# Optimization experiments

Hardware: AMD Instinct MI355X
Metric: run time of the kernel (lower is better)

The kernel has to match this reference:

```python
import jax, jax.numpy as jnp
import numpy as np

B, T, IN, D = 32, 1024, 1536, 768


def setup_inputs() -> dict:
    key = jax.random.key(0)
    ks = jax.random.split(key, 14)
    s_in = 1.0 / np.sqrt(IN)
    s_d = 1.0 / np.sqrt(D)
    return {
        "x": jax.random.normal(ks[0], (B, T, IN), jnp.float32),
        # fc1/fc2 torch Linear weights stored [out, in]
        "fc1_w": jax.random.normal(ks[1], (IN, IN), jnp.float32) * s_in,
        "fc1_b": jax.random.normal(ks[2], (IN,), jnp.float32) * 0.01,
        "fc2_w": jax.random.normal(ks[3], (D, IN), jnp.float32) * s_in,
        "fc2_b": jax.random.normal(ks[4], (D,), jnp.float32) * 0.01,
        # Unary: Conv1d(D,D,k=1) then Conv1d(D,1,k=1); k=1 conv == per-token linear
        "un_emb_w": jax.random.normal(ks[5], (D, D), jnp.float32) * s_d,
        "un_emb_b": jax.random.normal(ks[6], (D,), jnp.float32) * 0.01,
        "un_red_w": jax.random.normal(ks[7], (1, D), jnp.float32) * s_d,
        "un_red_b": jax.random.normal(ks[8], (1,), jnp.float32) * 0.01,
        # Self Pairwise: x_embedding / y_embedding Conv1d(D,D,k=1)
        "pw_x_w": jax.random.normal(ks[9], (D, D), jnp.float32) * s_d,
        "pw_x_b": jax.random.normal(ks[10], (D,), jnp.float32) * 0.01,
        "pw_y_w": jax.random.normal(ks[11], (D, D), jnp.float32) * s_d,
        "pw_y_b": jax.random.normal(ks[12], (D,), jnp.float32) * 0.01,
        # reduce_potentials: Conv1d(2,1,k=1,bias=False) -> 2 scalars
        "red_w": jax.random.normal(ks[13], (2,), jnp.float32),
    }


def reference(x, fc1_w, fc1_b, fc2_w, fc2_b,
              un_emb_w, un_emb_b, un_red_w, un_red_b,
              pw_x_w, pw_x_b, pw_y_w, pw_y_b, red_w):
    # FGAEmbedder MLP: fc2(relu(fc1(x)))
    h = jax.nn.relu(jnp.einsum('bti,oi->bto', x, fc1_w) + fc1_b)
    u = jnp.einsum('bti,oi->bto', h, fc2_w) + fc2_b            # [B,T,D]

    # Unary potential (dropout is identity at inference)
    e = jax.nn.relu(jnp.einsum('btd,od->bto', u, un_emb_w) + un_emb_b)
    un_pot = (jnp.einsum('btd,od->bto', e, un_red_w) + un_red_b)[..., 0]  # [B,T]

    # Self pairwise: cosine-similarity matrix, marginalized by mean (spatial_dim=None)
    xe = jnp.einsum('btd,od->bto', u, pw_x_w) + pw_x_b
    ye = jnp.einsum('btd,od->bto', u, pw_y_w) + pw_y_b
    xn = xe / jnp.maximum(jnp.linalg.norm(xe, axis=-1, keepdims=True), 1e-12)
    yn = ye / jnp.maximum(jnp.linalg.norm(ye, axis=-1, keepdims=True), 1e-12)
    S = jnp.einsum('btd,bsd->bts', xn, yn)                     # [B,T,T]
    pw_pot = jnp.mean(S, axis=2)                               # [B,T]

    # reduce potentials (Conv1d 2->1 no bias; order: unary then self), softmax attention
    scores = red_w[0] * un_pot + red_w[1] * pw_pot             # [B,T]
    w = jax.nn.softmax(scores, axis=1)
    return jnp.einsum('btd,bt->bd', u, w)                      # [B,D]
```

## Files before the change

### kernel.cpp

```cpp
#include <hip/hip_runtime.h>
#include <stdint.h>

#define MROWS 32768
#define TSEQ  1024
#define BBATCH 32
#define INDIM 1536
#define DDIM  768
#define NCAT  2304

typedef short short8 __attribute__((ext_vector_type(8)));
typedef short short4v __attribute__((ext_vector_type(4)));
typedef float f32x4  __attribute__((ext_vector_type(4)));

__device__ __forceinline__ float b2f(ushort u) {
    union { uint32_t u; float f; } x; x.u = ((uint32_t)u) << 16; return x.f;
}
__device__ __forceinline__ ushort f2b(float f) {
    union { float f; uint32_t u; } x; x.f = f;
    uint32_t r = x.u + 0x7fffu + ((x.u >> 16) & 1u);
    return (ushort)(r >> 16);
}

__device__ __forceinline__ void cvt4(const float* __restrict__ in, ushort* __restrict__ out, int i) {
    float4 v = ((const float4*)in)[i];
    ushort4 o;
    o.x = f2b(v.x); o.y = f2b(v.y); o.z = f2b(v.z); o.w = f2b(v.w);
    ((ushort4*)out)[i] = o;
}

#define C0 12582912
#define C1 13172736
#define C2 13467648
#define C3 13615104
#define C4 13762560
#define C5 13910016
#define C6 13910592
#define C7 13916736
#define C8 13922880
#define C9 13947456
__global__ void cvt_all(const float* __restrict__ x,
                        const float* __restrict__ fc1_w, const float* __restrict__ fc2_w,
                        const float* __restrict__ w3a, const float* __restrict__ w3b,
                        const float* __restrict__ w3c,
                        const float* __restrict__ ba, const float* __restrict__ bb,
                        const float* __restrict__ bc,
                        ushort* __restrict__ X16, ushort* __restrict__ W1,
                        ushort* __restrict__ W2, ushort* __restrict__ W3,
                        float* __restrict__ B3, float* __restrict__ ybar_z,
                        float* __restrict__ out_z, float* __restrict__ stats_z)
{
    int i = blockIdx.x * 256 + threadIdx.x;
    float4 z = {0.f, 0.f, 0.f, 0.f};
    if (i < C0)       cvt4(x, X16, i);
    else if (i < C1)  cvt4(fc1_w, W1, i - C0);
    else if (i < C2)  cvt4(fc2_w, W2, i - C1);
    else if (i < C3)  cvt4(w3a, W3,           i - C2);
    else if (i < C4)  cvt4(w3b, W3 + 589824,  i - C3);
    else if (i < C5)  cvt4(w3c, W3 + 1179648, i - C4);
    else if (i < C6) {
        int j = i - C5;
        const float* src = (j < 192) ? ba : (j < 384) ? bb : bc;
        int off = (j < 192) ? j : (j < 384) ? (j - 192) : (j - 384);
        ((float4*)B3)[j] = ((const float4*)src)[off];
    }
    else if (i < C7)  ((float4*)ybar_z)[i - C6] = z;
    else if (i < C8)  ((float4*)out_z)[i - C7] = z;
    else if (i < C9)  ((float4*)stats_z)[i - C8] = z;
}

__global__ __launch_bounds__(512, 2)
void gemm_bt(const ushort* __restrict__ A, const ushort* __restrict__ Bm,
             const float* __restrict__ bias, ushort* __restrict__ C,
             int M, int N, int K, int relu_ncols,
             const float* __restrict__ urw, float* __restrict__ SE,
             float* __restrict__ SX, float* __restrict__ SY)
{
    __shared__ __align__(16) ushort lds[81920];

    const int tid  = threadIdx.x;
    const int lane = tid & 63, wave = tid >> 6;
    const int wm = wave >> 2, wn = wave & 3;
    const int quad = lane >> 4, r16 = lane & 15;

    const int ntiles = N >> 8;
    const int xcd = blockIdx.x & 7;
    const int j   = blockIdx.x >> 3;
    const int g   = j / ntiles;
    const int n_t = j - g * ntiles;
    const int m_t = xcd + (g << 3);
    const int m0 = m_t * 256, n0 = n_t * 256;

    const int srow = lane >> 2;
    const int g8   = (((lane & 3) ^ ((srow >> 1) & 3)) << 3);
    const int goff = (r16 << 5) + ((quad ^ ((r16 >> 1) & 3)) << 3);

    const ushort* pA = A + (size_t)(m0 + (wave & 3) * 16 + srow + (wave >> 2) * 128) * K + g8;
    const int segA = (((wave >> 2) * 8 + (wave & 3)) << 9) + lane * 8;
    const ushort* pB = Bm + (size_t)(n0 + (wave >> 1) * 64 + (wave & 1) * 16 + srow) * K + g8;
    const int segB = (((wave >> 1) * 4 + (wave & 1)) << 9) + lane * 8;

    const int kT = K >> 6;

#define STG(p, off) __builtin_amdgcn_global_load_lds( \
        (const __attribute__((address_space(1))) void*)(p), \
        (__attribute__((address_space(3))) void*)&lds[off], 16, 0, 0)
#define STAGE_A(tt, MH) do { \
        const ushort* s_ = pA + (size_t)(MH) * 64 * K + (size_t)(tt) * 64; \
        const int d_ = ((tt) % 3) * 16384 + (MH) * 2048 + segA; \
        STG(s_,      d_); \
        STG(s_ + 32, d_ + 8192); } while (0)
#define STAGE_B(tt, NH) do { \
        const ushort* s_ = pB + (size_t)(NH) * 32 * K + (size_t)(tt) * 64; \
        const int d_ = 49152 + ((tt) & 1) * 16384 + (NH) * 1024 + segB; \
        STG(s_,      d_); \
        STG(s_ + 32, d_ + 8192); } while (0)

    STAGE_A(0, 0); STAGE_A(0, 1);
    STAGE_B(0, 0); STAGE_B(0, 1);
    STAGE_A(1, 0); STAGE_A(1, 1);
    asm volatile("s_waitcnt vmcnt(4)" ::: "memory");
    asm volatile("s_barrier" ::: "memory");

    f32x4 acc[8][4] = {};

    for (int t = 0; t < kT; ++t) {
        const int aB = (t % 3) * 16384;
        const int bB = 49152 + (t & 1) * 16384;
        short8 af0[2][4], af1[2][4], bf[2][4];

#pragma unroll
        for (int ks = 0; ks < 2; ++ks) {
#pragma unroll
            for (int i = 0; i < 4; ++i)
                af0[ks][i] = *(const short8*)&lds[aB + ks * 8192 + (wm * 8 + i) * 512 + goff];
#pragma unroll
            for (int jj = 0; jj < 4; ++jj)
                bf[ks][jj] = *(const short8*)&lds[bB + ks * 8192 + (wn * 4 + jj) * 512 + goff];
        }
        if (t + 1 < kT) { STAGE_B(t + 1, 0); STAGE_B(t + 1, 1); }
        if (t + 2 < kT) { STAGE_A(t + 2, 0); STAGE_A(t + 2, 1); }

        __builtin_amdgcn_s_setprio(1);
#pragma unroll
        for (int i = 0; i < 4; ++i)
#pragma unroll
            for (int jj = 0; jj < 4; ++jj) {
                acc[i][jj] = __builtin_amdgcn_mfma_f32_16x16x32_bf16(af0[0][i], bf[0][jj], acc[i][jj], 0, 0, 0);
                acc[i][jj] = __builtin_amdgcn_mfma_f32_16x16x32_bf16(af0[1][i], bf[1][jj], acc[i][jj], 0, 0, 0);
            }
        __builtin_amdgcn_s_setprio(0);

#pragma unroll
        for (int ks = 0; ks < 2; ++ks)
#pragma unroll
            for (int i = 0; i < 4; ++i)
                af1[ks][i] = *(const short8*)&lds[aB + ks * 8192 + (wm * 8 + 4 + i) * 512 + goff];

        __builtin_amdgcn_s_setprio(1);
#pragma unroll
        for (int i = 0; i < 4; ++i)
#pragma unroll
            for (int jj = 0; jj < 4; ++jj) {
                acc[4 + i][jj] = __builtin_amdgcn_mfma_f32_16x16x32_bf16(af1[0][i], bf[0][jj], acc[4 + i][jj], 0, 0, 0);
                acc[4 + i][jj] = __builtin_amdgcn_mfma_f32_16x16x32_bf16(af1[1][i], bf[1][jj], acc[4 + i][jj], 0, 0, 0);
            }
        __builtin_amdgcn_s_setprio(0);

        if (t + 2 < kT)      asm volatile("s_waitcnt vmcnt(4)" ::: "memory");
        else if (t + 1 < kT) asm volatile("s_waitcnt vmcnt(0)" ::: "memory");
        if (t + 1 < kT)      asm volatile("s_barrier" ::: "memory");
    }
#undef STAGE_A
#undef STAGE_B
#undef STG

    const bool stats = (urw != nullptr);
    const int sec = n0 / DDIM;
    float bv[4], uwv[4];
    bool dr[4];
#pragma unroll
    for (int jj = 0; jj < 4; ++jj) {
        int gn = n0 + wn * 64 + jj * 16 + r16;
        bv[jj] = bias[gn];
        dr[jj] = gn < relu_ncols;
        uwv[jj] = (stats && sec == 0) ? urw[gn] : 0.f;
    }
    float st[8][4] = {};
#pragma unroll
    for (int i = 0; i < 8; ++i) {
#pragma unroll
        for (int rr = 0; rr < 4; ++rr) {
            size_t base = (size_t)(m0 + wm * 128 + i * 16 + quad * 4 + rr) * N + n0 + wn * 64 + r16;
#pragma unroll
            for (int jj = 0; jj < 4; ++jj) {
                float v = acc[i][jj][rr] + bv[jj];
                if (dr[jj]) v = fmaxf(v, 0.f);
                C[base + jj * 16] = f2b(v);
                if (stats) st[i][rr] += (sec == 0) ? v * uwv[jj] : v * v;
            }
        }
    }
    if (stats) {
#pragma unroll
        for (int i = 0; i < 8; ++i)
#pragma unroll
            for (int rr = 0; rr < 4; ++rr) {
                float v = st[i][rr];
                v += __shfl_xor(v, 1, 64);
                v += __shfl_xor(v, 2, 64);
                v += __shfl_xor(v, 4, 64);
                v += __shfl_xor(v, 8, 64);
                st[i][rr] = v;
            }
        if (r16 == 0) {
            float* dst = (sec == 0) ? SE : (sec == 1) ? SX : SY;
#pragma unroll
            for (int i = 0; i < 8; ++i)
#pragma unroll
                for (int rr = 0; rr < 4; ++rr)
                    atomicAdd(&dst[m0 + wm * 128 + i * 16 + quad * 4 + rr], st[i][rr]);
        }
    }
}

__global__ void ybar_k(const ushort* __restrict__ G3, const float* __restrict__ sy,
                       float* __restrict__ ybar)
{
    int b = blockIdx.x, s0 = blockIdx.y * 32;
    int tid = threadIdx.x;
    __shared__ float sr[32];
    if (tid < 32) {
        float v = sy[b * TSEQ + s0 + tid];
        sr[tid] = (1.0f / TSEQ) / fmaxf(sqrtf(v), 1e-12f);
    }
    __syncthreads();
    float a0 = 0.f, a1 = 0.f, a2 = 0.f;
#pragma unroll 8
    for (int s = 0; s < 32; ++s) {
        const ushort* row = G3 + (size_t)(b * TSEQ + s0 + s) * NCAT + 2 * DDIM;
        float w = sr[s];
        a0 += b2f(row[tid])       * w;
        a1 += b2f(row[tid + 256]) * w;
        a2 += b2f(row[tid + 512]) * w;
    }
    atomicAdd(&ybar[b * DDIM + tid],       a0);
    atomicAdd(&ybar[b * DDIM + tid + 256], a1);
    atomicAdd(&ybar[b * DDIM + tid + 512], a2);
}

__global__ void pw_scores_k(const ushort* __restrict__ G3, const float* __restrict__ ybar,
                            const float* __restrict__ SE, const float* __restrict__ SX,
                            const float* __restrict__ urb, const float* __restrict__ red_w,
                            float* __restrict__ scores)
{
    int wv = threadIdx.x >> 6, lane = threadIdx.x & 63;
    int m = blockIdx.x * 4 + wv;
    int b = m >> 10;
    const ushort* xe = G3 + (size_t)m * NCAT + DDIM;
    const float4* yb = (const float4*)(ybar + b * DDIM);
    float s = 0.f;
#pragma unroll
    for (int c0 = 0; c0 < 3; ++c0) {
        int c = lane + c0 * 64;
        short4v v = *(const short4v*)(xe + c * 4);
        float4 yv = yb[c];
        s += b2f((ushort)v[0]) * yv.x + b2f((ushort)v[1]) * yv.y
           + b2f((ushort)v[2]) * yv.z + b2f((ushort)v[3]) * yv.w;
    }
#pragma unroll
    for (int off = 32; off; off >>= 1) s += __shfl_xor(s, off, 64);
    if (lane == 0) {
        float rnx = 1.f / fmaxf(sqrtf(SX[m]), 1e-12f);
        scores[m] = red_w[0] * (SE[m] + urb[0]) + red_w[1] * (rnx * s);
    }
}

__global__ void out_sm_k(const ushort* __restrict__ U16, const float* __restrict__ scores,
                         float* __restrict__ out)
{
    int b = blockIdx.x, t0 = blockIdx.y * 32;
    int tid = threadIdx.x;
    int lane = tid & 63, wv = tid >> 6;
    __shared__ float red[8];
    __shared__ float sw[32];

    float v[4];
    float lm = -1e30f;
#pragma unroll
    for (int i = 0; i < 4; ++i) {
        v[i] = scores[b * TSEQ + i * 256 + tid];
        lm = fmaxf(lm, v[i]);
    }
#pragma unroll
    for (int off = 32; off; off >>= 1) lm = fmaxf(lm, __shfl_xor(lm, off, 64));
    if (lane == 0) red[wv] = lm;
    __syncthreads();
    float smax = fmaxf(fmaxf(red[0], red[1]), fmaxf(red[2], red[3]));
    float ls = 0.f;
#pragma unroll
    for (int i = 0; i < 4; ++i) ls += expf(v[i] - smax);
#pragma unroll
    for (int off = 32; off; off >>= 1) ls += __shfl_xor(ls, off, 64);
    if (lane == 0) red[4 + wv] = ls;
    __syncthreads();
    float inv = 1.f / (red[4] + red[5] + red[6] + red[7]);

    if (tid < 32) sw[tid] = expf(scores[b * TSEQ + t0 + tid] - smax) * inv;
    __syncthreads();

    float a0 = 0.f, a1 = 0.f, a2 = 0.f;
#pragma unroll 8
    for (int t = 0; t < 32; ++t) {
        const ushort* row = U16 + (size_t)(b * TSEQ + t0 + t) * DDIM;
        float w = sw[t];
        a0 += b2f(row[tid])       * w;
        a1 += b2f(row[tid + 256]) * w;
        a2 += b2f(row[tid + 512]) * w;
    }
    atomicAdd(&out[b * DDIM + tid],       a0);
    atomicAdd(&out[b * DDIM + tid + 256], a1);
    atomicAdd(&out[b * DDIM + tid + 512], a2);
}

static const size_t O_X16   = 0;
static const size_t O_H16   = 100663296;
static const size_t O_G3    = 0;
static const size_t O_U16   = 201326592;
static const size_t O_W1    = 251658240;
static const size_t O_W2    = 256376832;
static const size_t O_W3    = 258736128;
static const size_t O_B3    = 262275072;
static const size_t O_SE    = 262284288;
static const size_t O_SX    = 262415360;
static const size_t O_SY    = 262546432;
static const size_t O_SCORE = 262677504;
static const size_t O_YBAR  = 262939648;

extern "C" void kernel_launch(void* const* d_in, const int* in_sizes, int n_in,
                              void* d_out, int out_size, void* d_ws, size_t ws_size,
                              hipStream_t stream)
{
    const float* x        = (const float*)d_in[0];
    const float* fc1_w    = (const float*)d_in[1];
    const float* fc1_b    = (const float*)d_in[2];
    const float* fc2_w    = (const float*)d_in[3];
    const float* fc2_b    = (const float*)d_in[4];
    const float* un_emb_w = (const float*)d_in[5];
    const float* un_emb_b = (const float*)d_in[6];
    const float* un_red_w = (const float*)d_in[7];
    const float* un_red_b = (const float*)d_in[8];
    const float* pw_x_w   = (const float*)d_in[9];
    const float* pw_x_b   = (const float*)d_in[10];
    const float* pw_y_w   = (const float*)d_in[11];
    const float* pw_y_b   = (const float*)d_in[12];
    const float* red_w    = (const float*)d_in[13];

    char* ws = (char*)d_ws;
    ushort* X16 = (ushort*)(ws + O_X16);
    ushort* H16 = (ushort*)(ws + O_H16);
    ushort* G3  = (ushort*)(ws + O_G3);
    ushort* U16 = (ushort*)(ws + O_U16);
    ushort* W1  = (ushort*)(ws + O_W1);
    ushort* W2  = (ushort*)(ws + O_W2);
    ushort* W3  = (ushort*)(ws + O_W3);
    float*  B3  = (float*)(ws + O_B3);
    float*  SE  = (float*)(ws + O_SE);
    float*  SX  = (float*)(ws + O_SX);
    float*  SY  = (float*)(ws + O_SY);
    float*  SCORES = (float*)(ws + O_SCORE);
    float*  YBAR = (float*)(ws + O_YBAR);

    cvt_all<<<54483, 256, 0, stream>>>(x, fc1_w, fc2_w, un_emb_w, pw_x_w, pw_y_w,
                                       un_emb_b, pw_x_b, pw_y_b,
                                       X16, W1, W2, W3, B3, YBAR, (float*)d_out, SE);

    gemm_bt<<<(MROWS / 256) * (INDIM / 256), 512, 0, stream>>>(
        X16, W1, fc1_b, H16, MROWS, INDIM, INDIM, INDIM,
        nullptr, nullptr, nullptr, nullptr);
    gemm_bt<<<(MROWS / 256) * (DDIM / 256), 512, 0, stream>>>(
        H16, W2, fc2_b, U16, MROWS, DDIM, INDIM, 0,
        nullptr, nullptr, nullptr, nullptr);
    gemm_bt<<<(MROWS / 256) * (NCAT / 256), 512, 0, stream>>>(
        U16, W3, B3, G3, MROWS, NCAT, DDIM, DDIM,
        un_red_w, SE, SX, SY);

    ybar_k<<<dim3(BBATCH, 32), 256, 0, stream>>>(G3, SY, YBAR);
    pw_scores_k<<<MROWS / 4, 256, 0, stream>>>(G3, YBAR, SE, SX, un_red_b, red_w, SCORES);
    out_sm_k<<<dim3(BBATCH, 32), 256, 0, stream>>>(U16, SCORES, (float*)d_out);
}
```

Baseline: 700.3 us.

## Reassociate pairwise projections through linearity to avoid storing G3 output

The third GEMM no longer writes its 32768x2304 bf16 output and only accumulates the per-row statistics (unary dot, x and y squared norms). The normalized-y mean is recomputed by projecting a norm-weighted mean of u through the fp32 y-weights. That result is folded back through the x-weights into a per-batch vector z and a bias term c1, so the pairwise score becomes a dot with u. This removes a large global store and the re-reads of G3, at the cost of several small extra kernels with naive fp32 matvecs and slightly different rounding, since the bf16 rounding of the projections is skipped.

```diff
diff --git a/kernel.cpp b/kernel.cpp
--- a/kernel.cpp
+++ b/kernel.cpp
@@ -28,16 +28,16 @@
     ((ushort4*)out)[i] = o;
 }
 
-#define C0 12582912
-#define C1 13172736
-#define C2 13467648
-#define C3 13615104
-#define C4 13762560
-#define C5 13910016
-#define C6 13910592
-#define C7 13916736
-#define C8 13922880
-#define C9 13947456
+#define CV0 12582912
+#define CV1 13172736
+#define CV2 13467648
+#define CV3 13615104
+#define CV4 13762560
+#define CV5 13910016
+#define CV6 13910592
+#define CV7 13916736
+#define CV8 13922880
+#define CV9 13947456
 __global__ void cvt_all(const float* __restrict__ x,
                         const float* __restrict__ fc1_w, const float* __restrict__ fc2_w,
                         const float* __restrict__ w3a, const float* __restrict__ w3b,
@@ -46,26 +46,26 @@
                         const float* __restrict__ bc,
                         ushort* __restrict__ X16, ushort* __restrict__ W1,
                         ushort* __restrict__ W2, ushort* __restrict__ W3,
-                        float* __restrict__ B3, float* __restrict__ ybar_z,
+                        float* __restrict__ B3, float* __restrict__ ubar_z,
                         float* __restrict__ out_z, float* __restrict__ stats_z)
 {
     int i = blockIdx.x * 256 + threadIdx.x;
     float4 z = {0.f, 0.f, 0.f, 0.f};
-    if (i < C0)       cvt4(x, X16, i);
-    else if (i < C1)  cvt4(fc1_w, W1, i - C0);
-    else if (i < C2)  cvt4(fc2_w, W2, i - C1);
-    else if (i < C3)  cvt4(w3a, W3,           i - C2);
-    else if (i < C4)  cvt4(w3b, W3 + 589824,  i - C3);
-    else if (i < C5)  cvt4(w3c, W3 + 1179648, i - C4);
-    else if (i < C6) {
-        int j = i - C5;
+    if (i < CV0)       cvt4(x, X16, i);
+    else if (i < CV1)  cvt4(fc1_w, W1, i - CV0);
+    else if (i < CV2)  cvt4(fc2_w, W2, i - CV1);
+    else if (i < CV3)  cvt4(w3a, W3,           i - CV2);
+    else if (i < CV4)  cvt4(w3b, W3 + 589824,  i - CV3);
+    else if (i < CV5)  cvt4(w3c, W3 + 1179648, i - CV4);
+    else if (i < CV6) {
+        int j = i - CV5;
         const float* src = (j < 192) ? ba : (j < 384) ? bb : bc;
         int off = (j < 192) ? j : (j < 384) ? (j - 192) : (j - 384);
         ((float4*)B3)[j] = ((const float4*)src)[off];
     }
-    else if (i < C7)  ((float4*)ybar_z)[i - C6] = z;
-    else if (i < C8)  ((float4*)out_z)[i - C7] = z;
-    else if (i < C9)  ((float4*)stats_z)[i - C8] = z;
+    else if (i < CV7)  ((float4*)ubar_z)[i - CV6] = z;
+    else if (i < CV8)  ((float4*)out_z)[i - CV7] = z;
+    else if (i < CV9)  ((float4*)stats_z)[i - CV8] = z;
 }
 
 __global__ __launch_bounds__(512, 2)
@@ -175,6 +175,7 @@
 #undef STG
 
     const bool stats = (urw != nullptr);
+    const bool dostore = (C != nullptr);
     const int sec = n0 / DDIM;
     float bv[4], uwv[4];
     bool dr[4];
@@ -195,7 +196,7 @@
             for (int jj = 0; jj < 4; ++jj) {
                 float v = acc[i][jj][rr] + bv[jj];
                 if (dr[jj]) v = fmaxf(v, 0.f);
-                C[base + jj * 16] = f2b(v);
+                if (dostore) C[base + jj * 16] = f2b(v);
                 if (stats) st[i][rr] += (sec == 0) ? v * uwv[jj] : v * v;
             }
         }
@@ -223,8 +224,20 @@
     }
 }
 
-__global__ void ybar_k(const ushort* __restrict__ G3, const float* __restrict__ sy,
-                       float* __restrict__ ybar)
+__global__ void sinv_k(const float* __restrict__ SY, float* __restrict__ Sinv)
+{
+    int b = blockIdx.x, lane = threadIdx.x;
+    float s = 0.f;
+#pragma unroll
+    for (int i = 0; i < TSEQ / 64; ++i)
+        s += 1.f / fmaxf(sqrtf(SY[b * TSEQ + lane + i * 64]), 1e-12f);
+#pragma unroll
+    for (int off = 32; off; off >>= 1) s += __shfl_xor(s, off, 64);
+    if (lane == 0) Sinv[b] = s * (1.0f / TSEQ);
+}
+
+__global__ void ubar_k(const ushort* __restrict__ U16, const float* __restrict__ sy,
+                       float* __restrict__ ubar)
 {
     int b = blockIdx.x, s0 = blockIdx.y * 32;
     int tid = threadIdx.x;
@@ -237,18 +250,56 @@
     float a0 = 0.f, a1 = 0.f, a2 = 0.f;
 #pragma unroll 8
     for (int s = 0; s < 32; ++s) {
-        const ushort* row = G3 + (size_t)(b * TSEQ + s0 + s) * NCAT + 2 * DDIM;
+        const ushort* row = U16 + (size_t)(b * TSEQ + s0 + s) * DDIM;
         float w = sr[s];
         a0 += b2f(row[tid])       * w;
         a1 += b2f(row[tid + 256]) * w;
         a2 += b2f(row[tid + 512]) * w;
     }
-    atomicAdd(&ybar[b * DDIM + tid],       a0);
-    atomicAdd(&ybar[b * DDIM + tid + 256], a1);
-    atomicAdd(&ybar[b * DDIM + tid + 512], a2);
-}
-
-__global__ void pw_scores_k(const ushort* __restrict__ G3, const float* __restrict__ ybar,
+    atomicAdd(&ubar[b * DDIM + tid],       a0);
+    atomicAdd(&ubar[b * DDIM + tid + 256], a1);
+    atomicAdd(&ubar[b * DDIM + tid + 512], a2);
+}
+
+__global__ void ybar_gemm(const float* __restrict__ Wy, const float* __restrict__ by,
+                          const float* __restrict__ ubar, const float* __restrict__ Sinv,
+                          float* __restrict__ ybar)
+{
+    int idx = blockIdx.x * 256 + threadIdx.x;
+    int o = idx >> 5, b = idx & 31;
+    const float* wr = Wy + (size_t)o * DDIM;
+    const float* ub = ubar + b * DDIM;
+    float s = 0.f;
+#pragma unroll 4
+    for (int i = 0; i < DDIM; ++i) s += wr[i] * ub[i];
+    ybar[b * DDIM + o] = s + by[o] * Sinv[b];
+}
+
+__global__ void c1_k(const float* __restrict__ bx, const float* __restrict__ ybar,
+                     float* __restrict__ c1)
+{
+    int b = blockIdx.x, lane = threadIdx.x;
+    float s = 0.f;
+#pragma unroll
+    for (int i = 0; i < DDIM / 64; ++i)
+        s += bx[lane + i * 64] * ybar[b * DDIM + lane + i * 64];
+#pragma unroll
+    for (int off = 32; off; off >>= 1) s += __shfl_xor(s, off, 64);
+    if (lane == 0) c1[b] = s;
+}
+
+__global__ void z_gemm(const float* __restrict__ Wx, const float* __restrict__ ybar,
+                       float* __restrict__ z)
+{
+    int b = blockIdx.x, i = blockIdx.y * 256 + threadIdx.x;
+    const float* yb = ybar + b * DDIM;
+    float s = 0.f;
+    for (int o = 0; o < DDIM; ++o) s += yb[o] * Wx[(size_t)o * DDIM + i];
+    z[b * DDIM + i] = s;
+}
+
+__global__ void pw_scores_k(const ushort* __restrict__ U16, const float* __restrict__ z,
+                            const float* __restrict__ c1,
                             const float* __restrict__ SE, const float* __restrict__ SX,
                             const float* __restrict__ urb, const float* __restrict__ red_w,
                             float* __restrict__ scores)
@@ -256,22 +307,22 @@
     int wv = threadIdx.x >> 6, lane = threadIdx.x & 63;
     int m = blockIdx.x * 4 + wv;
     int b = m >> 10;
-    const ushort* xe = G3 + (size_t)m * NCAT + DDIM;
-    const float4* yb = (const float4*)(ybar + b * DDIM);
+    const ushort* u = U16 + (size_t)m * DDIM;
+    const float4* zb = (const float4*)(z + b * DDIM);
     float s = 0.f;
 #pragma unroll
     for (int c0 = 0; c0 < 3; ++c0) {
         int c = lane + c0 * 64;
-        short4v v = *(const short4v*)(xe + c * 4);
-        float4 yv = yb[c];
-        s += b2f((ushort)v[0]) * yv.x + b2f((ushort)v[1]) * yv.y
-           + b2f((ushort)v[2]) * yv.z + b2f((ushort)v[3]) * yv.w;
+        short4v v = *(const short4v*)(u + c * 4);
+        float4 zv = zb[c];
+        s += b2f((ushort)v[0]) * zv.x + b2f((ushort)v[1]) * zv.y
+           + b2f((ushort)v[2]) * zv.z + b2f((ushort)v[3]) * zv.w;
     }
 #pragma unroll
     for (int off = 32; off; off >>= 1) s += __shfl_xor(s, off, 64);
     if (lane == 0) {
         float rnx = 1.f / fmaxf(sqrtf(SX[m]), 1e-12f);
-        scores[m] = red_w[0] * (SE[m] + urb[0]) + red_w[1] * (rnx * s);
+        scores[m] = red_w[0] * (SE[m] + urb[0]) + red_w[1] * ((s + c1[b]) * rnx);
     }
 }
 
@@ -324,7 +375,10 @@
 
 static const size_t O_X16   = 0;
 static const size_t O_H16   = 100663296;
-static const size_t O_G3    = 0;
+static const size_t O_YBR2  = 0;
+static const size_t O_Z     = 98304;
+static const size_t O_PC1   = 196608;
+static const size_t O_SINV  = 196736;
 static const size_t O_U16   = 201326592;
 static const size_t O_W1    = 251658240;
 static const size_t O_W2    = 256376832;
@@ -334,7 +388,7 @@
 static const size_t O_SX    = 262415360;
 static const size_t O_SY    = 262546432;
 static const size_t O_SCORE = 262677504;
-static const size_t O_YBAR  = 262939648;
+static const size_t O_UBAR  = 262939648;
 
 extern "C" void kernel_launch(void* const* d_in, const int* in_sizes, int n_in,
                               void* d_out, int out_size, void* d_ws, size_t ws_size,
@@ -358,7 +412,6 @@
     char* ws = (char*)d_ws;
     ushort* X16 = (ushort*)(ws + O_X16);
     ushort* H16 = (ushort*)(ws + O_H16);
-    ushort* G3  = (ushort*)(ws + O_G3);
     ushort* U16 = (ushort*)(ws + O_U16);
     ushort* W1  = (ushort*)(ws + O_W1);
     ushort* W2  = (ushort*)(ws + O_W2);
@@ -368,11 +421,15 @@
     float*  SX  = (float*)(ws + O_SX);
     float*  SY  = (float*)(ws + O_SY);
     float*  SCORES = (float*)(ws + O_SCORE);
-    float*  YBAR = (float*)(ws + O_YBAR);
+    float*  UBAR = (float*)(ws + O_UBAR);
+    float*  YBR2 = (float*)(ws + O_YBR2);
+    float*  Z    = (float*)(ws + O_Z);
+    float*  PC1  = (float*)(ws + O_PC1);
+    float*  SINV = (float*)(ws + O_SINV);
 
     cvt_all<<<54483, 256, 0, stream>>>(x, fc1_w, fc2_w, un_emb_w, pw_x_w, pw_y_w,
                                        un_emb_b, pw_x_b, pw_y_b,
-                                       X16, W1, W2, W3, B3, YBAR, (float*)d_out, SE);
+                                       X16, W1, W2, W3, B3, UBAR, (float*)d_out, SE);
 
     gemm_bt<<<(MROWS / 256) * (INDIM / 256), 512, 0, stream>>>(
         X16, W1, fc1_b, H16, MROWS, INDIM, INDIM, INDIM,
@@ -381,10 +438,14 @@
         H16, W2, fc2_b, U16, MROWS, DDIM, INDIM, 0,
         nullptr, nullptr, nullptr, nullptr);
     gemm_bt<<<(MROWS / 256) * (NCAT / 256), 512, 0, stream>>>(
-        U16, W3, B3, G3, MROWS, NCAT, DDIM, DDIM,
+        U16, W3, B3, nullptr, MROWS, NCAT, DDIM, DDIM,
         un_red_w, SE, SX, SY);
 
-    ybar_k<<<dim3(BBATCH, 32), 256, 0, stream>>>(G3, SY, YBAR);
-    pw_scores_k<<<MROWS / 4, 256, 0, stream>>>(G3, YBAR, SE, SX, un_red_b, red_w, SCORES);
+    sinv_k<<<BBATCH, 64, 0, stream>>>(SY, SINV);
+    ubar_k<<<dim3(BBATCH, 32), 256, 0, stream>>>(U16, SY, UBAR);
+    ybar_gemm<<<96, 256, 0, stream>>>(pw_y_w, pw_y_b, UBAR, SINV, YBR2);
+    c1_k<<<BBATCH, 64, 0, stream>>>(pw_x_b, YBR2, PC1);
+    z_gemm<<<dim3(BBATCH, 3), 256, 0, stream>>>(pw_x_w, YBR2, Z);
+    pw_scores_k<<<MROWS / 4, 256, 0, stream>>>(U16, Z, PC1, SE, SX, un_red_b, red_w, SCORES);
     out_sm_k<<<dim3(BBATCH, 32), 256, 0, stream>>>(U16, SCORES, (float*)d_out);
 }
```

After: 811.0 us. +15.8%, slower.
